# Optimization experiments

Hardware: AMD Instinct MI355X
Metric: run time of the kernel (lower is better)

The kernel has to match this reference:

```python
import jax, jax.numpy as jnp
import numpy as np

RANK_WEIGHT = 0.1  # init kwarg rank_weight
EPS = 1e-08


def setup_inputs() -> dict:
    key = jax.random.key(0)
    k1, k2, k3, k4 = jax.random.split(key, 4)
    B, D = 8192, 128
    return {
        "q_embeddings": jax.random.normal(k1, (B, D), dtype=jnp.float32),
        "a_embeddings": jax.random.normal(k2, (B, D), dtype=jnp.float32),
        "question_ids": jax.random.randint(k3, (B,), 0, 2048, dtype=jnp.int64),
        "ranks": jax.random.uniform(k4, (B,), dtype=jnp.float32),
    }


def reference(q_embeddings, a_embeddings, question_ids, ranks):
    # NOTE: the original computes q@a.T/temperature into `similarity` but the
    # per-sample loop recomputes sims WITHOUT temperature; we match the loop math.
    sims = jnp.matmul(q_embeddings, a_embeddings.T)  # [B, B]
    same_q = question_ids[:, None] == question_ids[None, :]  # [B, B] bool
    # pos_mask weight per positive column j: 1 - rank_weight * ranks[j]
    w = jnp.where(same_q, 1.0 - RANK_WEIGHT * ranks[None, :], 0.0)  # [B, B]
    # stable exp-ratio: sum(w*exp(s)) / sum(exp(s))
    m = jnp.max(sims, axis=1, keepdims=True)
    e = jnp.exp(sims - m)
    num = jnp.sum(w * e, axis=1)
    den = jnp.sum(e, axis=1)
    loss = jnp.mean(-jnp.log(num / den + EPS))
    pred = jnp.argmax(sims, axis=1)  # [B]
    correct = jnp.take_along_axis(w, pred[:, None], axis=1)[:, 0] > 0
    accuracy = jnp.mean(correct.astype(jnp.float32))
    return loss, accuracy
```

## Files before the change

kernel.cpp:

```cpp
#include <hip/hip_runtime.h>
#include <cmath>

#define B_N 8192
#define D_K 128
#define ROWS 128
#define CSPLIT 16
#define T_OUT 8

typedef float f32x4 __attribute__((ext_vector_type(4)));
typedef long  lx2   __attribute__((ext_vector_type(2)));

typedef __attribute__((address_space(3))) unsigned int as3_uint;
typedef __attribute__((address_space(1))) unsigned int as1_uint;

__device__ __forceinline__ void gl_lds16(const void* g, void* l) {
    __builtin_amdgcn_global_load_lds((const as1_uint*)(uintptr_t)g,
                                     (as3_uint*)(unsigned int)(uintptr_t)l,
                                     16, 0, 0);
}

__global__ void cvt_kernel(const float* __restrict__ q, const float* __restrict__ a,
                           unsigned char* __restrict__ qp, unsigned char* __restrict__ ap,
                           float* __restrict__ out) {
    const int g = blockIdx.x * blockDim.x + threadIdx.x;
    if (g < 2) out[g] = 0.0f;

    float4 q0 = reinterpret_cast<const float4*>(q)[g * 2];
    float4 q1 = reinterpret_cast<const float4*>(q)[g * 2 + 1];
    float4 a0 = reinterpret_cast<const float4*>(a)[g * 2];
    float4 a1 = reinterpret_cast<const float4*>(a)[g * 2 + 1];

    int qw0 = __builtin_amdgcn_cvt_pk_fp8_f32(q0.x, q0.y, 0, false);
    qw0     = __builtin_amdgcn_cvt_pk_fp8_f32(q0.z, q0.w, qw0, true);
    int qw1 = __builtin_amdgcn_cvt_pk_fp8_f32(q1.x, q1.y, 0, false);
    qw1     = __builtin_amdgcn_cvt_pk_fp8_f32(q1.z, q1.w, qw1, true);
    int aw0 = __builtin_amdgcn_cvt_pk_fp8_f32(a0.x, a0.y, 0, false);
    aw0     = __builtin_amdgcn_cvt_pk_fp8_f32(a0.z, a0.w, aw0, true);
    int aw1 = __builtin_amdgcn_cvt_pk_fp8_f32(a1.x, a1.y, 0, false);
    aw1     = __builtin_amdgcn_cvt_pk_fp8_f32(a1.z, a1.w, aw1, true);

    *reinterpret_cast<int2*>(qp + (size_t)g * 8) = make_int2(qw0, qw1);

    const int col = g >> 4, sq = g & 15;
    const int s = sq >> 2, quad = sq & 3;
    const int T = col >> 4, e = col & 15;
    const size_t off = (size_t)T * 2048 + (size_t)(s >> 1) * 1024
                     + (size_t)(quad * 16 + e) * 16 + (size_t)(s & 1) * 8;
    *reinterpret_cast<int2*>(ap + off) = make_int2(aw0, aw1);
}

__launch_bounds__(256, 4)
__global__ void mpl_part_kernel(const unsigned char* __restrict__ qp,
                                const unsigned char* __restrict__ ap,
                                const int* __restrict__ qids,
                                const float* __restrict__ ranks,
                                float* __restrict__ pden, float* __restrict__ pnum,
                                float* __restrict__ pmax, float* __restrict__ pmaxp) {
    __shared__ unsigned char smem[2 * 8192];

    const int tid  = threadIdx.x;
    const int lane = tid & 63;
    const int wave = tid >> 6;
    const int rg   = blockIdx.x >> 4;
    const int cs   = blockIdx.x & 15;
    const int rowBaseW = rg * ROWS + wave * 32;
    const int quad = lane >> 4;
    const int l15  = lane & 15;

    long qfragA[4], qfragB[4];
    {
        const unsigned char* qrowA = qp + (size_t)(rowBaseW + l15) * D_K + quad * 8;
        const unsigned char* qrowB = qrowA + 16 * D_K;
        #pragma unroll
        for (int s = 0; s < 4; ++s) {
            qfragA[s] = *reinterpret_cast<const long*>(qrowA + s * 32);
            qfragB[s] = *reinterpret_cast<const long*>(qrowB + s * 32);
        }
    }

    int qidrowA[4], qidrowB[4];
    #pragma unroll
    for (int r = 0; r < 4; ++r) {
        qidrowA[r] = qids[rowBaseW + quad * 4 + r];
        qidrowB[r] = qids[rowBaseW + 16 + quad * 4 + r];
    }

    float denA[4], numA[4], mxvA[4], mxpA[4];
    float denB[4], numB[4], mxvB[4], mxpB[4];
    #pragma unroll
    for (int r = 0; r < 4; ++r) {
        denA[r] = 0.f; numA[r] = 0.f; mxvA[r] = -INFINITY; mxpA[r] = -INFINITY;
        denB[r] = 0.f; numB[r] = 0.f; mxvB[r] = -INFINITY; mxpB[r] = -INFINITY;
    }

    const float L2E = 1.4426950408889634f;
    const float CB  = 64.0f;
    const int colStart = cs * 512;

    const char* gstrip = (const char*)ap + (size_t)cs * 65536;
    const int   chunk  = wave * 2048;

    #pragma unroll
    for (int i = 0; i < 2; ++i)
        gl_lds16(gstrip + chunk + i * 1024 + lane * 16,
                 (char*)smem + chunk + i * 1024);
    __syncthreads();

    for (int t = 0; t < T_OUT; ++t) {
        const int cur = t & 1, nxt = cur ^ 1;
        if (t + 1 < T_OUT) {
            const char* gsrc = gstrip + (size_t)(t + 1) * 8192 + chunk;
            char*       ldst = (char*)smem + nxt * 8192 + chunk;
            #pragma unroll
            for (int i = 0; i < 2; ++i)
                gl_lds16(gsrc + i * 1024 + lane * 16, ldst + i * 1024);
        }

        const unsigned char* lbase = smem + cur * 8192 + lane * 16;
        #pragma unroll
        for (int u = 0; u < 4; ++u) {
            lx2 b01 = *reinterpret_cast<const lx2*>(lbase + u * 2048);
            lx2 b23 = *reinterpret_cast<const lx2*>(lbase + u * 2048 + 1024);

            f32x4 accA = {0.f, 0.f, 0.f, 0.f};
            f32x4 accB = {0.f, 0.f, 0.f, 0.f};
            accA = __builtin_amdgcn_mfma_f32_16x16x32_fp8_fp8(qfragA[0], b01[0], accA, 0, 0, 0);
            accB = __builtin_amdgcn_mfma_f32_16x16x32_fp8_fp8(qfragB[0], b01[0], accB, 0, 0, 0);
            accA = __builtin_amdgcn_mfma_f32_16x16x32_fp8_fp8(qfragA[1], b01[1], accA, 0, 0, 0);
            accB = __builtin_amdgcn_mfma_f32_16x16x32_fp8_fp8(qfragB[1], b01[1], accB, 0, 0, 0);
            accA = __builtin_amdgcn_mfma_f32_16x16x32_fp8_fp8(qfragA[2], b23[0], accA, 0, 0, 0);
            accB = __builtin_amdgcn_mfma_f32_16x16x32_fp8_fp8(qfragB[2], b23[0], accB, 0, 0, 0);
            accA = __builtin_amdgcn_mfma_f32_16x16x32_fp8_fp8(qfragA[3], b23[1], accA, 0, 0, 0);
            accB = __builtin_amdgcn_mfma_f32_16x16x32_fp8_fp8(qfragB[3], b23[1], accB, 0, 0, 0);

            const int c  = colStart + t * 64 + u * 16 + l15;
            const int qc = qids[c];
            const float wc = 1.0f - 0.1f * ranks[c];
            #pragma unroll
            for (int r = 0; r < 4; ++r) {
                float sv = accA[r];
                float e  = __builtin_amdgcn_exp2f(fmaf(sv, L2E, -CB));
                bool pos = (qc == qidrowA[r]);
                denA[r] += e;
                numA[r] = fmaf(pos ? wc : 0.0f, e, numA[r]);
                mxvA[r] = fmaxf(mxvA[r], sv);
                mxpA[r] = fmaxf(mxpA[r], pos ? sv : -INFINITY);
            }
            #pragma unroll
            for (int r = 0; r < 4; ++r) {
                float sv = accB[r];
                float e  = __builtin_amdgcn_exp2f(fmaf(sv, L2E, -CB));
                bool pos = (qc == qidrowB[r]);
                denB[r] += e;
                numB[r] = fmaf(pos ? wc : 0.0f, e, numB[r]);
                mxvB[r] = fmaxf(mxvB[r], sv);
                mxpB[r] = fmaxf(mxpB[r], pos ? sv : -INFINITY);
            }
        }
        __syncthreads();
    }

    #pragma unroll
    for (int m = 1; m <= 8; m <<= 1) {
        #pragma unroll
        for (int r = 0; r < 4; ++r) {
            denA[r] += __shfl_xor(denA[r], m, 64);
            numA[r] += __shfl_xor(numA[r], m, 64);
            mxvA[r]  = fmaxf(mxvA[r], __shfl_xor(mxvA[r], m, 64));
            mxpA[r]  = fmaxf(mxpA[r], __shfl_xor(mxpA[r], m, 64));
            denB[r] += __shfl_xor(denB[r], m, 64);
            numB[r] += __shfl_xor(numB[r], m, 64);
            mxvB[r]  = fmaxf(mxvB[r], __shfl_xor(mxvB[r], m, 64));
            mxpB[r]  = fmaxf(mxpB[r], __shfl_xor(mxpB[r], m, 64));
        }
    }

    if (l15 == 0) {
        const int rb = cs * B_N + rowBaseW + quad * 4;
        #pragma unroll
        for (int r = 0; r < 4; ++r) {
            pden[rb + r]       = denA[r];
            pnum[rb + r]       = numA[r];
            pmax[rb + r]       = mxvA[r];
            pmaxp[rb + r]      = mxpA[r];
            pden[rb + 16 + r]  = denB[r];
            pnum[rb + 16 + r]  = numB[r];
            pmax[rb + 16 + r]  = mxvB[r];
            pmaxp[rb + 16 + r] = mxpB[r];
        }
    }
}

__launch_bounds__(256, 4)
__global__ void fin_kernel(const float* __restrict__ pden, const float* __restrict__ pnum,
                           const float* __restrict__ pmax, const float* __restrict__ pmaxp,
                           float* __restrict__ out) {
    const int r = blockIdx.x * 256 + threadIdx.x;
    float d = 0.f, n = 0.f, mv = -INFINITY, mp = -INFINITY;
    #pragma unroll
    for (int cs = 0; cs < CSPLIT; ++cs) {
        d += pden[cs * B_N + r];
        n += pnum[cs * B_N + r];
        mv = fmaxf(mv, pmax[cs * B_N + r]);
        mp = fmaxf(mp, pmaxp[cs * B_N + r]);
    }
    float lsum = -logf(n / d + 1e-8f);
    float csum = (mp == mv) ? 1.0f : 0.0f;
    #pragma unroll
    for (int m = 1; m <= 32; m <<= 1) {
        lsum += __shfl_xor(lsum, m, 64);
        csum += __shfl_xor(csum, m, 64);
    }
    __shared__ float sl[4], sc[4];
    const int wave = threadIdx.x >> 6;
    if ((threadIdx.x & 63) == 0) { sl[wave] = lsum; sc[wave] = csum; }
    __syncthreads();
    if (threadIdx.x == 0) {
        float L = sl[0] + sl[1] + sl[2] + sl[3];
        float C = sc[0] + sc[1] + sc[2] + sc[3];
        atomicAdd(&out[0], L * (1.0f / B_N));
        atomicAdd(&out[1], C * (1.0f / B_N));
    }
}

extern "C" void kernel_launch(void* const* d_in, const int* in_sizes, int n_in,
                              void* d_out, int out_size, void* d_ws, size_t ws_size,
                              hipStream_t stream) {
    const float* q     = (const float*)d_in[0];
    const float* a     = (const float*)d_in[1];
    const int*   qids  = (const int*)d_in[2];
    const float* ranks = (const float*)d_in[3];
    float* out = (float*)d_out;

    unsigned char* qp = (unsigned char*)d_ws;
    unsigned char* ap = qp + (size_t)B_N * D_K;
    char* p = (char*)(ap + (size_t)B_N * D_K);
    float* pden  = (float*)p;                p += CSPLIT * B_N * sizeof(float);
    float* pnum  = (float*)p;                p += CSPLIT * B_N * sizeof(float);
    float* pmax  = (float*)p;                p += CSPLIT * B_N * sizeof(float);
    float* pmaxp = (float*)p;

    cvt_kernel<<<(B_N * D_K / 8) / 256, 256, 0, stream>>>(q, a, qp, ap, out);
    mpl_part_kernel<<<(B_N / ROWS) * CSPLIT, 256, 0, stream>>>(qp, ap, qids, ranks,
                                                               pden, pnum, pmax, pmaxp);
    fin_kernel<<<B_N / 256, 256, 0, stream>>>(pden, pnum, pmax, pmaxp, out);
}
```

Baseline: 111.5 us.

## Drop LDS staging and load B fragments directly from global in smaller blocks

Removes the double-buffered global_load_lds staging of the packed answer strip and the per-tile barriers. Each wave now reads its MFMA B fragments straight from global memory (L2-cached) in one loop over 32 tiles. Blocks shrink from 4 waves to 2 waves (64 rows), doubling the grid, with no shared memory. This trades cross-wave reuse through LDS for no synchronisation and higher occupancy, but each wave now issues its own global loads, which raises L2 traffic.

```diff
diff --git a/kernel.cpp b/kernel.cpp
--- a/kernel.cpp
+++ b/kernel.cpp
@@ -3,21 +3,13 @@
 
 #define B_N 8192
 #define D_K 128
-#define ROWS 128
+#define WROWS 32
+#define BROWS 64
 #define CSPLIT 16
-#define T_OUT 8
+#define NTILE 32
 
 typedef float f32x4 __attribute__((ext_vector_type(4)));
 typedef long  lx2   __attribute__((ext_vector_type(2)));
-
-typedef __attribute__((address_space(3))) unsigned int as3_uint;
-typedef __attribute__((address_space(1))) unsigned int as1_uint;
-
-__device__ __forceinline__ void gl_lds16(const void* g, void* l) {
-    __builtin_amdgcn_global_load_lds((const as1_uint*)(uintptr_t)g,
-                                     (as3_uint*)(unsigned int)(uintptr_t)l,
-                                     16, 0, 0);
-}
 
 __global__ void cvt_kernel(const float* __restrict__ q, const float* __restrict__ a,
                            unsigned char* __restrict__ qp, unsigned char* __restrict__ ap,
@@ -49,21 +41,19 @@
     *reinterpret_cast<int2*>(ap + off) = make_int2(aw0, aw1);
 }
 
-__launch_bounds__(256, 4)
+__launch_bounds__(128, 4)
 __global__ void mpl_part_kernel(const unsigned char* __restrict__ qp,
                                 const unsigned char* __restrict__ ap,
                                 const int* __restrict__ qids,
                                 const float* __restrict__ ranks,
                                 float* __restrict__ pden, float* __restrict__ pnum,
                                 float* __restrict__ pmax, float* __restrict__ pmaxp) {
-    __shared__ unsigned char smem[2 * 8192];
-
     const int tid  = threadIdx.x;
     const int lane = tid & 63;
     const int wave = tid >> 6;
     const int rg   = blockIdx.x >> 4;
     const int cs   = blockIdx.x & 15;
-    const int rowBaseW = rg * ROWS + wave * 32;
+    const int rowBaseW = rg * BROWS + wave * WROWS;
     const int quad = lane >> 4;
     const int l15  = lane & 15;
 
@@ -97,67 +87,47 @@
     const float CB  = 64.0f;
     const int colStart = cs * 512;
 
-    const char* gstrip = (const char*)ap + (size_t)cs * 65536;
-    const int   chunk  = wave * 2048;
-
-    #pragma unroll
-    for (int i = 0; i < 2; ++i)
-        gl_lds16(gstrip + chunk + i * 1024 + lane * 16,
-                 (char*)smem + chunk + i * 1024);
-    __syncthreads();
-
-    for (int t = 0; t < T_OUT; ++t) {
-        const int cur = t & 1, nxt = cur ^ 1;
-        if (t + 1 < T_OUT) {
-            const char* gsrc = gstrip + (size_t)(t + 1) * 8192 + chunk;
-            char*       ldst = (char*)smem + nxt * 8192 + chunk;
-            #pragma unroll
-            for (int i = 0; i < 2; ++i)
-                gl_lds16(gsrc + i * 1024 + lane * 16, ldst + i * 1024);
-        }
-
-        const unsigned char* lbase = smem + cur * 8192 + lane * 16;
-        #pragma unroll
-        for (int u = 0; u < 4; ++u) {
-            lx2 b01 = *reinterpret_cast<const lx2*>(lbase + u * 2048);
-            lx2 b23 = *reinterpret_cast<const lx2*>(lbase + u * 2048 + 1024);
-
-            f32x4 accA = {0.f, 0.f, 0.f, 0.f};
-            f32x4 accB = {0.f, 0.f, 0.f, 0.f};
-            accA = __builtin_amdgcn_mfma_f32_16x16x32_fp8_fp8(qfragA[0], b01[0], accA, 0, 0, 0);
-            accB = __builtin_amdgcn_mfma_f32_16x16x32_fp8_fp8(qfragB[0], b01[0], accB, 0, 0, 0);
-            accA = __builtin_amdgcn_mfma_f32_16x16x32_fp8_fp8(qfragA[1], b01[1], accA, 0, 0, 0);
-            accB = __builtin_amdgcn_mfma_f32_16x16x32_fp8_fp8(qfragB[1], b01[1], accB, 0, 0, 0);
-            accA = __builtin_amdgcn_mfma_f32_16x16x32_fp8_fp8(qfragA[2], b23[0], accA, 0, 0, 0);
-            accB = __builtin_amdgcn_mfma_f32_16x16x32_fp8_fp8(qfragB[2], b23[0], accB, 0, 0, 0);
-            accA = __builtin_amdgcn_mfma_f32_16x16x32_fp8_fp8(qfragA[3], b23[1], accA, 0, 0, 0);
-            accB = __builtin_amdgcn_mfma_f32_16x16x32_fp8_fp8(qfragB[3], b23[1], accB, 0, 0, 0);
-
-            const int c  = colStart + t * 64 + u * 16 + l15;
-            const int qc = qids[c];
-            const float wc = 1.0f - 0.1f * ranks[c];
-            #pragma unroll
-            for (int r = 0; r < 4; ++r) {
-                float sv = accA[r];
-                float e  = __builtin_amdgcn_exp2f(fmaf(sv, L2E, -CB));
-                bool pos = (qc == qidrowA[r]);
-                denA[r] += e;
-                numA[r] = fmaf(pos ? wc : 0.0f, e, numA[r]);
-                mxvA[r] = fmaxf(mxvA[r], sv);
-                mxpA[r] = fmaxf(mxpA[r], pos ? sv : -INFINITY);
-            }
-            #pragma unroll
-            for (int r = 0; r < 4; ++r) {
-                float sv = accB[r];
-                float e  = __builtin_amdgcn_exp2f(fmaf(sv, L2E, -CB));
-                bool pos = (qc == qidrowB[r]);
-                denB[r] += e;
-                numB[r] = fmaf(pos ? wc : 0.0f, e, numB[r]);
-                mxvB[r] = fmaxf(mxvB[r], sv);
-                mxpB[r] = fmaxf(mxpB[r], pos ? sv : -INFINITY);
-            }
-        }
-        __syncthreads();
+    const char* strip = (const char*)ap + (size_t)cs * 65536 + lane * 16;
+
+    #pragma unroll 2
+    for (int u = 0; u < NTILE; ++u) {
+        lx2 b01 = *reinterpret_cast<const lx2*>(strip + u * 2048);
+        lx2 b23 = *reinterpret_cast<const lx2*>(strip + u * 2048 + 1024);
+
+        f32x4 accA = {0.f, 0.f, 0.f, 0.f};
+        f32x4 accB = {0.f, 0.f, 0.f, 0.f};
+        accA = __builtin_amdgcn_mfma_f32_16x16x32_fp8_fp8(qfragA[0], b01[0], accA, 0, 0, 0);
+        accB = __builtin_amdgcn_mfma_f32_16x16x32_fp8_fp8(qfragB[0], b01[0], accB, 0, 0, 0);
+        accA = __builtin_amdgcn_mfma_f32_16x16x32_fp8_fp8(qfragA[1], b01[1], accA, 0, 0, 0);
+        accB = __builtin_amdgcn_mfma_f32_16x16x32_fp8_fp8(qfragB[1], b01[1], accB, 0, 0, 0);
+        accA = __builtin_amdgcn_mfma_f32_16x16x32_fp8_fp8(qfragA[2], b23[0], accA, 0, 0, 0);
+        accB = __builtin_amdgcn_mfma_f32_16x16x32_fp8_fp8(qfragB[2], b23[0], accB, 0, 0, 0);
+        accA = __builtin_amdgcn_mfma_f32_16x16x32_fp8_fp8(qfragA[3], b23[1], accA, 0, 0, 0);
+        accB = __builtin_amdgcn_mfma_f32_16x16x32_fp8_fp8(qfragB[3], b23[1], accB, 0, 0, 0);
+
+        const int c  = colStart + u * 16 + l15;
+        const int qc = qids[c];
+        const float wc = 1.0f - 0.1f * ranks[c];
+        #pragma unroll
+        for (int r = 0; r < 4; ++r) {
+            float sv = accA[r];
+            float e  = __builtin_amdgcn_exp2f(fmaf(sv, L2E, -CB));
+            bool pos = (qc == qidrowA[r]);
+            denA[r] += e;
+            numA[r] = fmaf(pos ? wc : 0.0f, e, numA[r]);
+            mxvA[r] = fmaxf(mxvA[r], sv);
+            mxpA[r] = fmaxf(mxpA[r], pos ? sv : -INFINITY);
+        }
+        #pragma unroll
+        for (int r = 0; r < 4; ++r) {
+            float sv = accB[r];
+            float e  = __builtin_amdgcn_exp2f(fmaf(sv, L2E, -CB));
+            bool pos = (qc == qidrowB[r]);
+            denB[r] += e;
+            numB[r] = fmaf(pos ? wc : 0.0f, e, numB[r]);
+            mxvB[r] = fmaxf(mxvB[r], sv);
+            mxpB[r] = fmaxf(mxpB[r], pos ? sv : -INFINITY);
+        }
     }
 
     #pragma unroll
@@ -241,7 +211,7 @@
     float* pmaxp = (float*)p;
 
     cvt_kernel<<<(B_N * D_K / 8) / 256, 256, 0, stream>>>(q, a, qp, ap, out);
-    mpl_part_kernel<<<(B_N / ROWS) * CSPLIT, 256, 0, stream>>>(qp, ap, qids, ranks,
-                                                               pden, pnum, pmax, pmaxp);
+    mpl_part_kernel<<<(B_N / BROWS) * CSPLIT, 128, 0, stream>>>(qp, ap, qids, ranks,
+                                                                pden, pnum, pmax, pmaxp);
     fin_kernel<<<B_N / 256, 256, 0, stream>>>(pden, pnum, pmax, pmaxp, out);
 }
```

Result: faster. 107.9 us (-3.2%).

## Widen column strips per block, batch column metadata loads, split MFMA accumulators

Applied to the files above, without the earlier changes.

Halves the number of column splits so each block processes 1024 columns with 128-column tiles, doubling the LDS double-buffer to 32 KB. Per-tile qid/rank loads are hoisted into an 8-entry batch before the MFMA loop, and each dot product is split across two independent accumulator chains to shorten the MFMA dependency chain. Fewer blocks means fewer partial results to reduce, but the larger LDS footprint and register use may reduce occupancy. The partial-output indexing in the unseen epilogue and the cvt layout may also need to match the new split.

```diff
diff --git a/kernel.cpp b/kernel.cpp
--- a/kernel.cpp
+++ b/kernel.cpp
@@ -4,7 +4,7 @@
 #define B_N 8192
 #define D_K 128
 #define ROWS 128
-#define CSPLIT 16
+#define CSPLIT 8
 #define T_OUT 8
 
 typedef float f32x4 __attribute__((ext_vector_type(4)));
@@ -56,13 +56,13 @@
                                 const float* __restrict__ ranks,
                                 float* __restrict__ pden, float* __restrict__ pnum,
                                 float* __restrict__ pmax, float* __restrict__ pmaxp) {
-    __shared__ unsigned char smem[2 * 8192];
+    __shared__ unsigned char smem[2 * 16384];
 
     const int tid  = threadIdx.x;
     const int lane = tid & 63;
     const int wave = tid >> 6;
-    const int rg   = blockIdx.x >> 4;
-    const int cs   = blockIdx.x & 15;
+    const int rg   = blockIdx.x >> 3;
+    const int cs   = blockIdx.x & 7;
     const int rowBaseW = rg * ROWS + wave * 32;
     const int quad = lane >> 4;
     const int l15  = lane & 15;
@@ -95,13 +95,13 @@
 
     const float L2E = 1.4426950408889634f;
     const float CB  = 64.0f;
-    const int colStart = cs * 512;
-
-    const char* gstrip = (const char*)ap + (size_t)cs * 65536;
-    const int   chunk  = wave * 2048;
-
-    #pragma unroll
-    for (int i = 0; i < 2; ++i)
+    const int colStart = cs * 1024;
+
+    const char* gstrip = (const char*)ap + (size_t)cs * 131072;
+    const int   chunk  = wave * 4096;
+
+    #pragma unroll
+    for (int i = 0; i < 4; ++i)
         gl_lds16(gstrip + chunk + i * 1024 + lane * 16,
                  (char*)smem + chunk + i * 1024);
     __syncthreads();
@@ -109,36 +109,46 @@
     for (int t = 0; t < T_OUT; ++t) {
         const int cur = t & 1, nxt = cur ^ 1;
         if (t + 1 < T_OUT) {
-            const char* gsrc = gstrip + (size_t)(t + 1) * 8192 + chunk;
-            char*       ldst = (char*)smem + nxt * 8192 + chunk;
+            const char* gsrc = gstrip + (size_t)(t + 1) * 16384 + chunk;
+            char*       ldst = (char*)smem + nxt * 16384 + chunk;
             #pragma unroll
-            for (int i = 0; i < 2; ++i)
+            for (int i = 0; i < 4; ++i)
                 gl_lds16(gsrc + i * 1024 + lane * 16, ldst + i * 1024);
         }
 
-        const unsigned char* lbase = smem + cur * 8192 + lane * 16;
-        #pragma unroll
-        for (int u = 0; u < 4; ++u) {
+        int   qc8[8];
+        float wc8[8];
+        #pragma unroll
+        for (int u = 0; u < 8; ++u) {
+            const int c = colStart + t * 128 + u * 16 + l15;
+            qc8[u] = qids[c];
+            wc8[u] = 1.0f - 0.1f * ranks[c];
+        }
+
+        const unsigned char* lbase = smem + cur * 16384 + lane * 16;
+        #pragma unroll
+        for (int u = 0; u < 8; ++u) {
             lx2 b01 = *reinterpret_cast<const lx2*>(lbase + u * 2048);
             lx2 b23 = *reinterpret_cast<const lx2*>(lbase + u * 2048 + 1024);
 
-            f32x4 accA = {0.f, 0.f, 0.f, 0.f};
-            f32x4 accB = {0.f, 0.f, 0.f, 0.f};
-            accA = __builtin_amdgcn_mfma_f32_16x16x32_fp8_fp8(qfragA[0], b01[0], accA, 0, 0, 0);
-            accB = __builtin_amdgcn_mfma_f32_16x16x32_fp8_fp8(qfragB[0], b01[0], accB, 0, 0, 0);
-            accA = __builtin_amdgcn_mfma_f32_16x16x32_fp8_fp8(qfragA[1], b01[1], accA, 0, 0, 0);
-            accB = __builtin_amdgcn_mfma_f32_16x16x32_fp8_fp8(qfragB[1], b01[1], accB, 0, 0, 0);
-            accA = __builtin_amdgcn_mfma_f32_16x16x32_fp8_fp8(qfragA[2], b23[0], accA, 0, 0, 0);
-            accB = __builtin_amdgcn_mfma_f32_16x16x32_fp8_fp8(qfragB[2], b23[0], accB, 0, 0, 0);
-            accA = __builtin_amdgcn_mfma_f32_16x16x32_fp8_fp8(qfragA[3], b23[1], accA, 0, 0, 0);
-            accB = __builtin_amdgcn_mfma_f32_16x16x32_fp8_fp8(qfragB[3], b23[1], accB, 0, 0, 0);
-
-            const int c  = colStart + t * 64 + u * 16 + l15;
-            const int qc = qids[c];
-            const float wc = 1.0f - 0.1f * ranks[c];
+            f32x4 accA1 = {0.f, 0.f, 0.f, 0.f};
+            f32x4 accA2 = {0.f, 0.f, 0.f, 0.f};
+            f32x4 accB1 = {0.f, 0.f, 0.f, 0.f};
+            f32x4 accB2 = {0.f, 0.f, 0.f, 0.f};
+            accA1 = __builtin_amdgcn_mfma_f32_16x16x32_fp8_fp8(qfragA[0], b01[0], accA1, 0, 0, 0);
+            accB1 = __builtin_amdgcn_mfma_f32_16x16x32_fp8_fp8(qfragB[0], b01[0], accB1, 0, 0, 0);
+            accA2 = __builtin_amdgcn_mfma_f32_16x16x32_fp8_fp8(qfragA[2], b23[0], accA2, 0, 0, 0);
+            accB2 = __builtin_amdgcn_mfma_f32_16x16x32_fp8_fp8(qfragB[2], b23[0], accB2, 0, 0, 0);
+            accA1 = __builtin_amdgcn_mfma_f32_16x16x32_fp8_fp8(qfragA[1], b01[1], accA1, 0, 0, 0);
+            accB1 = __builtin_amdgcn_mfma_f32_16x16x32_fp8_fp8(qfragB[1], b01[1], accB1, 0, 0, 0);
+            accA2 = __builtin_amdgcn_mfma_f32_16x16x32_fp8_fp8(qfragA[3], b23[1], accA2, 0, 0, 0);
+            accB2 = __builtin_amdgcn_mfma_f32_16x16x32_fp8_fp8(qfragB[3], b23[1], accB2, 0, 0, 0);
+
+            const int   qc = qc8[u];
+            const float wc = wc8[u];
             #pragma unroll
             for (int r = 0; r < 4; ++r) {
-                float sv = accA[r];
+                float sv = accA1[r] + accA2[r];
                 float e  = __builtin_amdgcn_exp2f(fmaf(sv, L2E, -CB));
                 bool pos = (qc == qidrowA[r]);
                 denA[r] += e;
@@ -148,7 +158,7 @@
             }
             #pragma unroll
             for (int r = 0; r < 4; ++r) {
-                float sv = accB[r];
+                float sv = accB1[r] + accB2[r];
                 float e  = __builtin_amdgcn_exp2f(fmaf(sv, L2E, -CB));
                 bool pos = (qc == qidrowB[r]);
                 denB[r] += e;
```

After: 143.8 us. +29.0%, slower.
